# Optimization experiments

Measured on AMD Instinct MI355X. Metric: run time of the kernel, lower is better.

The kernel has to match this reference:

```python
import jax, jax.numpy as jnp
import numpy as np

GAMMA = 2.6
SIG0, SIG1 = 0.17, 4.86
EXP_S, EXP_F = 2.0, 0.6

F1_NP = np.array([[0.0025, 0.0125, 0.02, 0.0125, 0.0025],
                  [0.0125, 0.0625, 0.1, 0.0625, 0.0125],
                  [0.02, 0.1, 0.16, 0.1, 0.02],
                  [0.0125, 0.0625, 0.1, 0.0625, 0.0125],
                  [0.0025, 0.0125, 0.02, 0.0125, 0.0025]], dtype=np.float32)[None, None]
FILT0_NP = np.array([[0.04, 0.04, 0.05, 0.04, 0.04],
                     [0.04, 0.03, 0.04, 0.03, 0.04],
                     [0.05, 0.04, 0.05, 0.04, 0.05],
                     [0.04, 0.03, 0.04, 0.03, 0.04],
                     [0.04, 0.04, 0.05, 0.04, 0.04]], dtype=np.float32)[None, None]
FILT1_NP = np.zeros((5, 5), dtype=np.float32)
FILT1_NP[2, 2] = 1.0
FILT1_NP = FILT1_NP[None, None]


def _pad_rep(x, p):
    return jnp.pad(x, ((0, 0), (0, 0), (p, p), (p, p)), mode='edge')


def _conv(x, f, pad=0):
    return jax.lax.conv_general_dilated(
        x, f, window_strides=(1, 1), padding=[(pad, pad), (pad, pad)],
        dimension_numbers=('NCHW', 'OIHW', 'NCHW'))


def _down(img, f):
    # replicate-pad by 2, valid 5x5 conv (output same HxW), stride-2 subsample
    o = _conv(_pad_rep(img, 2), f)
    return o[:, :, ::2, ::2]


def _up(img, odd, f):
    x = _pad_rep(img, 1)
    B, C, Hp, Wp = x.shape
    h, w = 2 * Hp, 2 * Wp
    o = jnp.zeros((B, C, h, w), x.dtype).at[:, :, ::2, ::2].set(4.0 * x)
    o = _conv(o, f, pad=2)
    return o[:, :, 2:h - 2 - odd[0], 2:w - 2 - odd[1]]


def _laplacian_pyramid(img, n_lev, f):
    pyr = []
    o = img
    for _ in range(n_lev - 1):
        g = _down(o, f)
        odd = [g.shape[2] * 2 - o.shape[2], g.shape[3] * 2 - o.shape[3]]
        pyr.append(o - _up(g, odd, f))
        o = g
    pyr.append(o)
    return pyr


def _nlp(img, n_lev, F1, filt0, filt1):
    img = img ** (1.0 / GAMMA)
    pyr = _laplacian_pyramid(img, n_lev, F1)
    npyr = []
    for i in range(n_lev - 1):
        den = _conv(_pad_rep(jnp.abs(pyr[i]), 2), filt0) + SIG0
        npyr.append(pyr[i] / den)
    den = _conv(_pad_rep(jnp.abs(pyr[-1]), 2), filt1) + SIG1
    npyr.append(pyr[-1] / den)
    return npyr


def setup_inputs() -> dict:
    key = jax.random.key(0)
    k1, k2 = jax.random.split(key)
    B, H, W = 16, 512, 512
    h_img = jax.random.uniform(k1, (B, 1, H, W), dtype=jnp.float32)
    l_img = jax.random.uniform(k2, (B, 1, H, W), dtype=jnp.float32)
    return {
        'h_img': h_img,
        'l_img': l_img,
        'F1': jnp.asarray(F1_NP),
        'filt0': jnp.asarray(FILT0_NP),
        'filt1': jnp.asarray(FILT1_NP),
        'n_lev': 7,
    }


def reference(h_img, l_img, F1, filt0, filt1, n_lev):
    h_pyr = _nlp(h_img, n_lev, F1, filt0, filt1)
    l_pyr = _nlp(l_img, n_lev, F1, filt0, filt1)
    dis = []
    for i in range(n_lev):
        diff = jnp.abs(h_pyr[i] - l_pyr[i]) ** EXP_S
        dis.append(jnp.mean(diff, axis=(-2, -1)) ** (EXP_F / EXP_S))  # [B, 1]
    dis = jnp.concatenate(dis, axis=-1)  # [B, n_lev]
    loss = jnp.mean(dis, axis=-1) ** (1.0 / EXP_F)
    return jnp.mean(loss)
```

## Files before the change

kernel.cpp:

```cpp
#include <hip/hip_runtime.h>

#define SIG0 0.17f
#define SIG1 4.86f

__device__ __constant__ float c_filt0[25] = {
  0.04f,0.04f,0.05f,0.04f,0.04f,
  0.04f,0.03f,0.04f,0.03f,0.04f,
  0.05f,0.04f,0.05f,0.04f,0.05f,
  0.04f,0.03f,0.04f,0.03f,0.04f,
  0.04f,0.04f,0.05f,0.04f,0.04f};
__device__ __constant__ float c_f1d[5] = {0.05f,0.25f,0.4f,0.25f,0.05f};

static __device__ __forceinline__ int iclamp(int v, int lo, int hi){
  return v < lo ? lo : (v > hi ? hi : v);
}

#define D0W 136
#define D0H 36
__global__ __launch_bounds__(256)
void down0_gamma(const float* __restrict__ hin, const float* __restrict__ lin,
                 float* __restrict__ g0, float* __restrict__ g1){
  const int H=512, W=512, Wo=256;
  int xo0 = blockIdx.x*64, yo0 = blockIdx.y*16;
  int z = blockIdx.z;
  const float* in = (z<16) ? (hin + (size_t)z*H*W) : (lin + (size_t)(z-16)*H*W);
  int tid = threadIdx.x;
  __shared__ float st[D0H][D0W];
  __shared__ float hs[D0H][64];
  const float e = 0.3846153846153846f;
  for (int f=tid; f<D0H*D0W; f+=256){
    int r=f/D0W, c=f%D0W;
    int yy=iclamp(2*yo0-2+r,0,H-1);
    int xx=iclamp(2*xo0-4+c,0,W-1);
    st[r][c] = __powf(in[(size_t)yy*W+xx], e);
  }
  __syncthreads();
  float* g0p = g0 + (size_t)z*H*W;
  for (int f=tid; f<32*32; f+=256){
    int r=f>>5, q=f&31;
    float4 v = *(const float4*)&st[2+r][4+4*q];
    *(float4*)&g0p[(size_t)(2*yo0+r)*W + 2*xo0 + 4*q] = v;
  }
  for (int f=tid; f<D0H*64; f+=256){
    int r=f>>6, xo=f&63;
    const float* rp = &st[r][2*xo+2];
    hs[r][xo] = 0.05f*rp[0]+0.25f*rp[1]+0.4f*rp[2]+0.25f*rp[3]+0.05f*rp[4];
  }
  __syncthreads();
  float* g1p = g1 + (size_t)z*Wo*Wo;
  for (int f=tid; f<16*64; f+=256){
    int yo=f>>6, xo=f&63;
    g1p[(size_t)(yo0+yo)*Wo + xo0+xo] =
      0.05f*hs[2*yo][xo]+0.25f*hs[2*yo+1][xo]+0.4f*hs[2*yo+2][xo]
     +0.25f*hs[2*yo+3][xo]+0.05f*hs[2*yo+4][xo];
  }
}

#define DTW 132
#define DTH 36
__global__ __launch_bounds__(256)
void down_kernel(const float* __restrict__ in, float* __restrict__ out,
                 int H, int W, int Ho, int Wo){
  int xo0 = blockIdx.x*64, yo0 = blockIdx.y*16, b = blockIdx.z;
  int tid = threadIdx.x;
  __shared__ float st[DTH][DTW];
  __shared__ float hs[DTH][64];
  const float* ip = in + (size_t)b*H*W;
  for (int f = tid; f < DTH*DTW; f += 256){
    int r = f / DTW, c = f % DTW;
    int yy = iclamp(2*yo0 - 2 + r, 0, H-1);
    int xx = iclamp(2*xo0 - 2 + c, 0, W-1);
    st[r][c] = ip[(size_t)yy*W + xx];
  }
  __syncthreads();
  for (int f = tid; f < DTH*64; f += 256){
    int r = f >> 6, xo = f & 63;
    const float* rp = st[r] + 2*xo;
    hs[r][xo] = 0.05f*rp[0] + 0.25f*rp[1] + 0.4f*rp[2] + 0.25f*rp[3] + 0.05f*rp[4];
  }
  __syncthreads();
  for (int f = tid; f < 16*64; f += 256){
    int yo = f >> 6, xo = f & 63;
    int X = xo0 + xo, Y = yo0 + yo;
    if (X < Wo && Y < Ho){
      out[(size_t)b*Ho*Wo + (size_t)Y*Wo + X] =
        0.05f*hs[2*yo][xo] + 0.25f*hs[2*yo+1][xo] + 0.4f*hs[2*yo+2][xo]
      + 0.25f*hs[2*yo+3][xo] + 0.05f*hs[2*yo+4][xo];
    }
  }
}

#define FTW 72
#define FTH 20
#define FGW 40
#define FGH 12

static __device__ __forceinline__ float4 rowi(const float* p){
  float4 t;
  t.x = 0.05f*p[0] + 0.4f*p[1] + 0.05f*p[2];
  t.y = 0.25f*(p[1]+p[2]);
  t.z = 0.05f*p[1] + 0.4f*p[2] + 0.05f*p[3];
  t.w = 0.25f*(p[2]+p[3]);
  return t;
}

__global__ __launch_bounds__(256)
void fused_kernel(const float* __restrict__ g0, const float* __restrict__ g1,
                  float* __restrict__ accum, int H, int W, int lev){
  int Hg=H>>1, Wg=W>>1;
  int x0 = blockIdx.x*64, y0 = blockIdx.y*16, b = blockIdx.z;
  int tid = threadIdx.x;
  bool edge = (blockIdx.x==0) || (blockIdx.x==gridDim.x-1) ||
              (blockIdx.y==0) || (blockIdx.y==gridDim.y-1);

  __shared__ float sg[2][FTH][FTW];
  __shared__ float s1[2][FGH][FGW];
  __shared__ float swave[4];

  const float* g0b0 = g0 + (size_t)b*H*W;
  const float* g0b1 = g0 + (size_t)(b+16)*H*W;
  const float* g1b0 = g1 + (size_t)b*Hg*Wg;
  const float* g1b1 = g1 + (size_t)(b+16)*Hg*Wg;
  int gy0 = (y0>>1)-2, gx0 = (x0>>1)-4;

  if (!edge){
    for (int f=tid; f<2*FTH*18; f+=256){
      int img=f/360, rem=f%360, r=rem/18, q=rem%18;
      const float* src = img ? g0b1 : g0b0;
      *(float4*)&sg[img][r][4*q] = *(const float4*)&src[(size_t)(y0-2+r)*W + x0-4+4*q];
    }
    for (int f=tid; f<2*FGH*10; f+=256){
      int img=f/120, rem=f%120, r=rem/10, q=rem%10;
      const float* src = img ? g1b1 : g1b0;
      *(float4*)&s1[img][r][4*q] = *(const float4*)&src[(size_t)(gy0+r)*Wg + gx0+4*q];
    }
    __syncthreads();
    for (int f=tid; f<2*FTH*18; f+=256){
      int img=f/360, rem=f%360, r=rem/18, q=rem%18;
      int ry = ((r-2)>>1) + 2;
      int cb = 2*q+1;
      float4 u;
      if ((r&1)==0){
        float4 a = rowi(&s1[img][ry-1][cb]);
        float4 m = rowi(&s1[img][ry  ][cb]);
        float4 c2 = rowi(&s1[img][ry+1][cb]);
        u.x = 0.2f*a.x + 1.6f*m.x + 0.2f*c2.x;
        u.y = 0.2f*a.y + 1.6f*m.y + 0.2f*c2.y;
        u.z = 0.2f*a.z + 1.6f*m.z + 0.2f*c2.z;
        u.w = 0.2f*a.w + 1.6f*m.w + 0.2f*c2.w;
      } else {
        float4 a = rowi(&s1[img][ry  ][cb]);
        float4 m = rowi(&s1[img][ry+1][cb]);
        u.x = a.x + m.x; u.y = a.y + m.y; u.z = a.z + m.z; u.w = a.w + m.w;
      }
      float4 val = *(float4*)&sg[img][r][4*q];
      val.x -= u.x; val.y -= u.y; val.z -= u.z; val.w -= u.w;
      *(float4*)&sg[img][r][4*q] = val;
    }
  } else {
    for (int f=tid; f<2*FTH*FTW; f+=256){
      int img=f/(FTH*FTW), rem=f%(FTH*FTW), r=rem/FTW, c=rem%FTW;
      int yy=iclamp(y0-2+r,0,H-1), xx=iclamp(x0-4+c,0,W-1);
      const float* src = img ? g0b1 : g0b0;
      sg[img][r][c] = src[(size_t)yy*W+xx];
    }
    for (int f=tid; f<2*FGH*FGW; f+=256){
      int img=f/(FGH*FGW), rem=f%(FGH*FGW), r=rem/FGW, c=rem%FGW;
      int yy=iclamp(gy0+r,0,Hg-1), xx=iclamp(gx0+c,0,Wg-1);
      const float* src = img ? g1b1 : g1b0;
      s1[img][r][c] = src[(size_t)yy*Wg+xx];
    }
    __syncthreads();
    for (int f=tid; f<2*FTH*FTW; f+=256){
      int img=f/(FTH*FTW), rem=f%(FTH*FTW), r=rem/FTW, c=rem%FTW;
      int yy=iclamp(y0-2+r,0,H-1), xx=iclamp(x0-4+c,0,W-1);
      int y2=yy>>1, x2=xx>>1;
      int ry0,ry1,ry2; float wy0,wy1,wy2;
      if ((yy&1)==0){
        ry0=iclamp(y2-1,0,Hg-1); ry1=y2; ry2=iclamp(y2+1,0,Hg-1);
        wy0=0.2f; wy1=1.6f; wy2=0.2f;
      } else {
        ry0=y2; ry1=iclamp(y2+1,0,Hg-1); ry2=y2;
        wy0=1.0f; wy1=1.0f; wy2=0.0f;
      }
      int cx0,cx1,cx2; float wx0,wx1,wx2;
      if ((xx&1)==0){
        cx0=iclamp(x2-1,0,Wg-1); cx1=x2; cx2=iclamp(x2+1,0,Wg-1);
        wx0=0.05f; wx1=0.4f; wx2=0.05f;
      } else {
        cx0=x2; cx1=iclamp(x2+1,0,Wg-1); cx2=x2;
        wx0=0.25f; wx1=0.25f; wx2=0.0f;
      }
      ry0-=gy0; ry1-=gy0; ry2-=gy0; cx0-=gx0; cx1-=gx0; cx2-=gx0;
      const float (*sp)[FGW] = s1[img];
      float u0 = wx0*sp[ry0][cx0] + wx1*sp[ry0][cx1] + wx2*sp[ry0][cx2];
      float u1 = wx0*sp[ry1][cx0] + wx1*sp[ry1][cx1] + wx2*sp[ry1][cx2];
      float u2 = wx0*sp[ry2][cx0] + wx1*sp[ry2][cx1] + wx2*sp[ry2][cx2];
      sg[img][r][c] -= wy0*u0 + wy1*u1 + wy2*u2;
    }
  }
  __syncthreads();

  int tx = tid & 15, ty = tid >> 4;
  int xl = tx*4;
  float denh[4], denl[4], numh[4], numl[4];
  #pragma unroll
  for (int j=0;j<4;j++){ denh[j]=SIG0; denl[j]=SIG0; }
  #pragma unroll
  for (int i=0;i<5;i++){
    float r_[12];
    *(float4*)&r_[0] = *(const float4*)&sg[0][ty+i][xl];
    *(float4*)&r_[4] = *(const float4*)&sg[0][ty+i][xl+4];
    *(float4*)&r_[8] = *(const float4*)&sg[0][ty+i][xl+8];
    if (i==2){ numh[0]=r_[4]; numh[1]=r_[5]; numh[2]=r_[6]; numh[3]=r_[7]; }
    #pragma unroll
    for (int jj=0;jj<5;jj++){
      float w = c_filt0[i*5+jj];
      #pragma unroll
      for (int j=0;j<4;j++) denh[j] += w*fabsf(r_[2+j+jj]);
    }
  }
  #pragma unroll
  for (int i=0;i<5;i++){
    float r_[12];
    *(float4*)&r_[0] = *(const float4*)&sg[1][ty+i][xl];
    *(float4*)&r_[4] = *(const float4*)&sg[1][ty+i][xl+4];
    *(float4*)&r_[8] = *(const float4*)&sg[1][ty+i][xl+8];
    if (i==2){ numl[0]=r_[4]; numl[1]=r_[5]; numl[2]=r_[6]; numl[3]=r_[7]; }
    #pragma unroll
    for (int jj=0;jj<5;jj++){
      float w = c_filt0[i*5+jj];
      #pragma unroll
      for (int j=0;j<4;j++) denl[j] += w*fabsf(r_[2+j+jj]);
    }
  }
  float v = 0.f;
  #pragma unroll
  for (int j=0;j<4;j++){
    float d = __fdividef(numh[j], denh[j]) - __fdividef(numl[j], denl[j]);
    v += d*d;
  }
  #pragma unroll
  for (int off=32; off>0; off>>=1) v += __shfl_down(v, off);
  if ((tid & 63) == 0) swave[tid>>6] = v;
  __syncthreads();
  if (tid == 0){
    float s = swave[0]+swave[1]+swave[2]+swave[3];
    atomicAdd(&accum[lev*16 + b], s);
  }
}

static __device__ __forceinline__ void down_lds(const float* Ain, int ldi, int Sin,
                                                float* Aout, int ldo, int Sout,
                                                int tid, int NT){
  int tot = 2*Sout*Sout;
  for (int f=tid; f<tot; f+=NT){
    int img = f/(Sout*Sout), rem = f%(Sout*Sout), y=rem/Sout, x=rem%Sout;
    const float* A = Ain + img*Sin*ldi;
    float s=0.f;
    #pragma unroll
    for (int i=0;i<5;i++){
      int yy=iclamp(2*y+i-2,0,Sin-1);
      float rs=0.f;
      #pragma unroll
      for (int j=0;j<5;j++){
        int xx=iclamp(2*x+j-2,0,Sin-1);
        rs += c_f1d[j]*A[yy*ldi+xx];
      }
      s += c_f1d[i]*rs;
    }
    Aout[img*Sout*ldo + y*ldo + x] = s;
  }
}

static __device__ __forceinline__ void lap_lds(float* Ak, int ldk, int S,
                                               const float* Ag, int ldg,
                                               int tid, int NT){
  int Sg = S>>1;
  int tot = 2*S*S;
  for (int f=tid; f<tot; f+=NT){
    int img=f/(S*S), rem=f%(S*S), y=rem/S, x=rem%S;
    const float* G = Ag + img*Sg*ldg;
    int y2=y>>1, x2=x>>1;
    int ry0,ry1,ry2; float wy0,wy1,wy2;
    if (!(y&1)){ ry0=iclamp(y2-1,0,Sg-1); ry1=y2; ry2=iclamp(y2+1,0,Sg-1); wy0=0.2f; wy1=1.6f; wy2=0.2f; }
    else { ry0=y2; ry1=iclamp(y2+1,0,Sg-1); ry2=y2; wy0=1.f; wy1=1.f; wy2=0.f; }
    int cx0,cx1,cx2; float wx0,wx1,wx2;
    if (!(x&1)){ cx0=iclamp(x2-1,0,Sg-1); cx1=x2; cx2=iclamp(x2+1,0,Sg-1); wx0=0.05f; wx1=0.4f; wx2=0.05f; }
    else { cx0=x2; cx1=iclamp(x2+1,0,Sg-1); cx2=x2; wx0=0.25f; wx1=0.25f; wx2=0.f; }
    float u0 = wx0*G[ry0*ldg+cx0]+wx1*G[ry0*ldg+cx1]+wx2*G[ry0*ldg+cx2];
    float u1 = wx0*G[ry1*ldg+cx0]+wx1*G[ry1*ldg+cx1]+wx2*G[ry1*ldg+cx2];
    float u2 = wx0*G[ry2*ldg+cx0]+wx1*G[ry2*ldg+cx1]+wx2*G[ry2*ldg+cx2];
    Ak[img*S*ldk + y*ldk + x] -= wy0*u0+wy1*u1+wy2*u2;
  }
}

static __device__ __forceinline__ float diff_lds(const float* A, int ld, int S,
                                                 int tid, int NT){
  float v=0.f;
  const float* Ah = A;
  const float* Al = A + S*ld;
  for (int f=tid; f<S*S; f+=NT){
    int y=f/S, x=f%S;
    float dh=SIG0, dl=SIG0;
    #pragma unroll
    for (int i=0;i<5;i++){
      int yy=iclamp(y+i-2,0,S-1);
      #pragma unroll
      for (int j=0;j<5;j++){
        int xx=iclamp(x+j-2,0,S-1);
        float w=c_filt0[i*5+j];
        dh += w*fabsf(Ah[yy*ld+xx]);
        dl += w*fabsf(Al[yy*ld+xx]);
      }
    }
    float d = __fdividef(Ah[y*ld+x],dh) - __fdividef(Al[y*ld+x],dl);
    v += d*d;
  }
  return v;
}

__global__ __launch_bounds__(512)
void tail_kernel(const float* __restrict__ g3, float* __restrict__ accum){
  const int NT = 512;
  int b = blockIdx.x;
  int tid = threadIdx.x;
  __shared__ float A3[2][64][66];
  __shared__ float A4[2][32][34];
  __shared__ float A5[2][16][18];
  __shared__ float A6[2][8][10];
  __shared__ float sred[8];

  const float* s0 = g3 + (size_t)b*4096;
  const float* s1p = g3 + (size_t)(b+16)*4096;
  for (int f=tid; f<2*4096; f+=NT){
    int img=f>>12, rem=f&4095, r=rem>>6, c=rem&63;
    A3[img][r][c] = img ? s1p[rem] : s0[rem];
  }
  __syncthreads();
  down_lds(&A3[0][0][0], 66, 64, &A4[0][0][0], 34, 32, tid, NT);
  __syncthreads();
  down_lds(&A4[0][0][0], 34, 32, &A5[0][0][0], 18, 16, tid, NT);
  __syncthreads();
  down_lds(&A5[0][0][0], 18, 16, &A6[0][0][0], 10, 8, tid, NT);
  __syncthreads();
  lap_lds(&A3[0][0][0], 66, 64, &A4[0][0][0], 34, tid, NT);
  __syncthreads();
  float v3 = diff_lds(&A3[0][0][0], 66, 64, tid, NT);
  lap_lds(&A4[0][0][0], 34, 32, &A5[0][0][0], 18, tid, NT);
  __syncthreads();
  float v4 = diff_lds(&A4[0][0][0], 34, 32, tid, NT);
  lap_lds(&A5[0][0][0], 18, 16, &A6[0][0][0], 10, tid, NT);
  __syncthreads();
  float v5 = diff_lds(&A5[0][0][0], 18, 16, tid, NT);
  float v6 = 0.f;
  for (int f=tid; f<64; f+=NT){
    float ch = A6[0][f>>3][f&7];
    float cl = A6[1][f>>3][f&7];
    float d = __fdividef(ch, fabsf(ch)+SIG1) - __fdividef(cl, fabsf(cl)+SIG1);
    v6 += d*d;
  }
  float vs[4] = {v3, v4, v5, v6};
  #pragma unroll
  for (int k=0;k<4;k++){
    float v = vs[k];
    #pragma unroll
    for (int off=32; off>0; off>>=1) v += __shfl_down(v, off);
    if ((tid&63)==0) sred[tid>>6] = v;
    __syncthreads();
    if (tid==0){
      float s=0.f;
      #pragma unroll
      for (int w=0;w<8;w++) s += sred[w];
      accum[(3+k)*16 + b] = s;
    }
    __syncthreads();
  }
}

__global__ __launch_bounds__(64)
void finalize_kernel(const float* __restrict__ accum, float* __restrict__ out){
  __shared__ float s[16];
  int b = threadIdx.x;
  if (b < 16){
    float m = 0.f;
    #pragma unroll
    for (int k=0;k<7;k++){
      int hw = (512>>k)*(512>>k);
      float mean = accum[k*16+b] / (float)hw;
      m += powf(mean, 0.3f);
    }
    m *= (1.0f/7.0f);
    s[b] = powf(m, 1.6666666666666667f);
  }
  __syncthreads();
  if (b == 0){
    float t = 0.f;
    #pragma unroll
    for (int i=0;i<16;i++) t += s[i];
    out[0] = t * (1.0f/16.0f);
  }
}

extern "C" void kernel_launch(void* const* d_in, const int* in_sizes, int n_in,
                              void* d_out, int out_size, void* d_ws, size_t ws_size,
                              hipStream_t stream){
  const float* h = (const float*)d_in[0];
  const float* l = (const float*)d_in[1];
  float* out = (float*)d_out;
  float* ws = (float*)d_ws;

  size_t off0 = 0;
  size_t off1 = off0 + (size_t)32*512*512;
  size_t off2 = off1 + (size_t)32*256*256;
  size_t off3 = off2 + (size_t)32*128*128;
  size_t offA = off3 + (size_t)32*64*64;
  float* accum = ws + offA;

  hipMemsetAsync(accum, 0, 112*sizeof(float), stream);

  down0_gamma<<<dim3(4,16,32), 256, 0, stream>>>(h, l, ws+off0, ws+off1);
  fused_kernel<<<dim3(8,32,16), 256, 0, stream>>>(ws+off0, ws+off1, accum, 512, 512, 0);
  down_kernel<<<dim3(2,8,32), 256, 0, stream>>>(ws+off1, ws+off2, 256, 256, 128, 128);
  fused_kernel<<<dim3(4,16,16), 256, 0, stream>>>(ws+off1, ws+off2, accum, 256, 256, 1);
  down_kernel<<<dim3(1,4,32), 256, 0, stream>>>(ws+off2, ws+off3, 128, 128, 64, 64);
  fused_kernel<<<dim3(2,8,16), 256, 0, stream>>>(ws+off2, ws+off3, accum, 128, 128, 2);
  tail_kernel<<<dim3(16), 512, 0, stream>>>(ws+off3, accum);
  finalize_kernel<<<1, 64, 0, stream>>>(accum, out);
}
```

Baseline: 195.5 us.

## Fuse pyramid stages into fewer launches with pre-padded buffers and recomputed level0

Drops the full-resolution gamma-corrected buffer g0 and recomputes the gamma power from the inputs inside the level-0 Laplacian kernel. Downsampled levels are stored with replicated-edge padding, so the fused kernels need no clamped slow path. Each downsample is merged into the same launch as the previous level's Laplacian/normalisation work using blockIdx.z partitioning, cutting the launch count from eight to five. Fused tiles grow to 32 rows, each thread computing two output rows. The cost is redundant pow evaluations, scattered halo writes and larger shared memory per block.

```diff
diff --git a/kernel.cpp b/kernel.cpp
--- a/kernel.cpp
+++ b/kernel.cpp
@@ -15,239 +15,244 @@
   return v < lo ? lo : (v > hi ? hi : v);
 }
 
-#define D0W 136
-#define D0H 36
-__global__ __launch_bounds__(256)
-void down0_gamma(const float* __restrict__ hin, const float* __restrict__ lin,
-                 float* __restrict__ g0, float* __restrict__ g1){
-  const int H=512, W=512, Wo=256;
-  int xo0 = blockIdx.x*64, yo0 = blockIdx.y*16;
-  int z = blockIdx.z;
-  const float* in = (z<16) ? (hin + (size_t)z*H*W) : (lin + (size_t)(z-16)*H*W);
-  int tid = threadIdx.x;
-  __shared__ float st[D0H][D0W];
-  __shared__ float hs[D0H][64];
-  const float e = 0.3846153846153846f;
-  for (int f=tid; f<D0H*D0W; f+=256){
-    int r=f/D0W, c=f%D0W;
-    int yy=iclamp(2*yo0-2+r,0,H-1);
-    int xx=iclamp(2*xo0-4+c,0,W-1);
-    st[r][c] = __powf(in[(size_t)yy*W+xx], e);
-  }
-  __syncthreads();
-  float* g0p = g0 + (size_t)z*H*W;
-  for (int f=tid; f<32*32; f+=256){
-    int r=f>>5, q=f&31;
-    float4 v = *(const float4*)&st[2+r][4+4*q];
-    *(float4*)&g0p[(size_t)(2*yo0+r)*W + 2*xo0 + 4*q] = v;
-  }
-  for (int f=tid; f<D0H*64; f+=256){
+
+struct FS {
+  float sg[2][36][76];
+  float s1[2][20][44];
+  float red[4];
+};
+struct DS {
+  float st[36][136];
+  float hs[36][64];
+};
+struct TS {
+  float A3[2][64][66];
+  float A4[2][32][34];
+  float A5[2][16][18];
+  float A6[2][8][10];
+  float red[4];
+};
+
+__device__ __forceinline__ void down_body(const float* __restrict__ in0, float* __restrict__ out0,
+                                          int PSI, int PSO, int Sout, int xo0, int yo0, char* smem){
+  DS* S = (DS*)smem;
+  int tid = threadIdx.x;
+  for (int f=tid; f<36*34; f+=256){
+    int r=f/34, c4=f%34;
+    *(float4*)&S->st[r][4*c4] = *(const float4*)&in0[(size_t)(2*yo0+r)*PSI + 2*xo0 + 4*c4];
+  }
+  __syncthreads();
+  for (int f=tid; f<36*64; f+=256){
     int r=f>>6, xo=f&63;
-    const float* rp = &st[r][2*xo+2];
-    hs[r][xo] = 0.05f*rp[0]+0.25f*rp[1]+0.4f*rp[2]+0.25f*rp[3]+0.05f*rp[4];
-  }
-  __syncthreads();
-  float* g1p = g1 + (size_t)z*Wo*Wo;
+    const float* rp = &S->st[r][2*xo+2];
+    S->hs[r][xo] = 0.05f*rp[0]+0.25f*rp[1]+0.4f*rp[2]+0.25f*rp[3]+0.05f*rp[4];
+  }
+  __syncthreads();
   for (int f=tid; f<16*64; f+=256){
     int yo=f>>6, xo=f&63;
-    g1p[(size_t)(yo0+yo)*Wo + xo0+xo] =
-      0.05f*hs[2*yo][xo]+0.25f*hs[2*yo+1][xo]+0.4f*hs[2*yo+2][xo]
-     +0.25f*hs[2*yo+3][xo]+0.05f*hs[2*yo+4][xo];
-  }
-}
-
-#define DTW 132
-#define DTH 36
+    int Y=yo0+yo, X=xo0+xo;
+    float v = 0.05f*S->hs[2*yo][xo]+0.25f*S->hs[2*yo+1][xo]+0.4f*S->hs[2*yo+2][xo]
+            +0.25f*S->hs[2*yo+3][xo]+0.05f*S->hs[2*yo+4][xo];
+    int rlo=(Y==0)?0:(Y+2), rhi=(Y==Sout-1)?(Sout+3):(Y+2);
+    int clo=(X==0)?0:(X+4), chi=(X==Sout-1)?(Sout+7):(X+4);
+    for (int rr=rlo; rr<=rhi; rr++)
+      for (int cc=clo; cc<=chi; cc++)
+        out0[(size_t)rr*PSO+cc] = v;
+  }
+}
+
 __global__ __launch_bounds__(256)
-void down_kernel(const float* __restrict__ in, float* __restrict__ out,
-                 int H, int W, int Ho, int Wo){
-  int xo0 = blockIdx.x*64, yo0 = blockIdx.y*16, b = blockIdx.z;
-  int tid = threadIdx.x;
-  __shared__ float st[DTH][DTW];
-  __shared__ float hs[DTH][64];
-  const float* ip = in + (size_t)b*H*W;
-  for (int f = tid; f < DTH*DTW; f += 256){
-    int r = f / DTW, c = f % DTW;
-    int yy = iclamp(2*yo0 - 2 + r, 0, H-1);
-    int xx = iclamp(2*xo0 - 2 + c, 0, W-1);
-    st[r][c] = ip[(size_t)yy*W + xx];
-  }
-  __syncthreads();
-  for (int f = tid; f < DTH*64; f += 256){
-    int r = f >> 6, xo = f & 63;
-    const float* rp = st[r] + 2*xo;
-    hs[r][xo] = 0.05f*rp[0] + 0.25f*rp[1] + 0.4f*rp[2] + 0.25f*rp[3] + 0.05f*rp[4];
-  }
-  __syncthreads();
-  for (int f = tid; f < 16*64; f += 256){
-    int yo = f >> 6, xo = f & 63;
-    int X = xo0 + xo, Y = yo0 + yo;
-    if (X < Wo && Y < Ho){
-      out[(size_t)b*Ho*Wo + (size_t)Y*Wo + X] =
-        0.05f*hs[2*yo][xo] + 0.25f*hs[2*yo+1][xo] + 0.4f*hs[2*yo+2][xo]
-      + 0.25f*hs[2*yo+3][xo] + 0.05f*hs[2*yo+4][xo];
-    }
-  }
-}
-
-#define FTW 72
-#define FTH 20
-#define FGW 40
-#define FGH 12
-
-static __device__ __forceinline__ float4 rowi(const float* p){
+void k_d1(const float* __restrict__ hin, const float* __restrict__ lin,
+          float* __restrict__ g1){
+  __shared__ DS S;
+  int xo0 = blockIdx.x*64, yo0 = blockIdx.y*16, z = blockIdx.z;
+  const float* in = (z<16)? hin + (size_t)z*262144 : lin + (size_t)(z-16)*262144;
+  float* out0 = g1 + (size_t)z*68640;
+  int tid = threadIdx.x;
+  const float e = 0.3846153846153846f;
+  for (int f=tid; f<36*34; f+=256){
+    int r=f/34, c4=f%34;
+    int yy = iclamp(2*yo0-2+r, 0, 511);
+    int xb = 2*xo0-4+4*c4;
+    const float* rp = in + (size_t)yy*512;
+    float4 v;
+    if (xb>=0 && xb<=508) v = *(const float4*)&rp[xb];
+    else { v.x=rp[iclamp(xb,0,511)]; v.y=rp[iclamp(xb+1,0,511)];
+           v.z=rp[iclamp(xb+2,0,511)]; v.w=rp[iclamp(xb+3,0,511)]; }
+    v.x=__powf(v.x,e); v.y=__powf(v.y,e); v.z=__powf(v.z,e); v.w=__powf(v.w,e);
+    *(float4*)&S.st[r][4*c4] = v;
+  }
+  __syncthreads();
+  for (int f=tid; f<36*64; f+=256){
+    int r=f>>6, xo=f&63;
+    const float* rp = &S.st[r][2*xo+2];
+    S.hs[r][xo] = 0.05f*rp[0]+0.25f*rp[1]+0.4f*rp[2]+0.25f*rp[3]+0.05f*rp[4];
+  }
+  __syncthreads();
+  for (int f=tid; f<16*64; f+=256){
+    int yo=f>>6, xo=f&63;
+    int Y=yo0+yo, X=xo0+xo;
+    float v = 0.05f*S.hs[2*yo][xo]+0.25f*S.hs[2*yo+1][xo]+0.4f*S.hs[2*yo+2][xo]
+            +0.25f*S.hs[2*yo+3][xo]+0.05f*S.hs[2*yo+4][xo];
+    int rlo=(Y==0)?0:(Y+2), rhi=(Y==255)?259:(Y+2);
+    int clo=(X==0)?0:(X+4), chi=(X==255)?263:(X+4);
+    for (int rr=rlo; rr<=rhi; rr++)
+      for (int cc=clo; cc<=chi; cc++)
+        out0[(size_t)rr*264+cc] = v;
+  }
+}
+
+__device__ __forceinline__ void fused_stage_s1(FS* S, const float* __restrict__ g10,
+                                               const float* __restrict__ g11,
+                                               int PS1, int x0, int y0){
+  int tid = threadIdx.x;
+  for (int f=tid; f<2*20*10; f+=256){
+    int img=f/200, rem=f%200, ro=rem/10, co=rem%10;
+    const float* src = img? g11 : g10;
+    *(float4*)&S->s1[img][ro][4*co] = *(const float4*)&src[(size_t)(y0/2+ro)*PS1 + x0/2 + 4*co];
+  }
+}
+
+__device__ __forceinline__ void fused_stage_g(FS* S, const float* __restrict__ gk0,
+                                              const float* __restrict__ gk1,
+                                              int PS0, int x0, int y0){
+  int tid = threadIdx.x;
+  for (int f=tid; f<2*36*18; f+=256){
+    int img=f/648, rem=f%648, r=rem/18, q=rem%18;
+    const float* src = img? gk1 : gk0;
+    *(float4*)&S->sg[img][r][4*q] = *(const float4*)&src[(size_t)(y0+r)*PS0 + x0 + 4*q];
+  }
+}
+
+__device__ __forceinline__ void fused_stage_in(FS* S, const float* __restrict__ h0,
+                                               const float* __restrict__ l0,
+                                               int x0, int y0){
+  int tid = threadIdx.x;
+  const float e = 0.3846153846153846f;
+  for (int f=tid; f<2*36*18; f+=256){
+    int img=f/648, rem=f%648, r=rem/18, q=rem%18;
+    const float* src = img? l0 : h0;
+    int yy = iclamp(y0-2+r, 0, 511);
+    int xb = x0-4+4*q;
+    const float* rp = src + (size_t)yy*512;
+    float4 v;
+    if (xb>=0 && xb<=508) v = *(const float4*)&rp[xb];
+    else { v.x=rp[iclamp(xb,0,511)]; v.y=rp[iclamp(xb+1,0,511)];
+           v.z=rp[iclamp(xb+2,0,511)]; v.w=rp[iclamp(xb+3,0,511)]; }
+    v.x=__powf(v.x,e); v.y=__powf(v.y,e); v.z=__powf(v.z,e); v.w=__powf(v.w,e);
+    *(float4*)&S->sg[img][r][4*q] = v;
+  }
+}
+
+__device__ __forceinline__ float4 up_row(const float* __restrict__ p){
+  float2 A = *(const float2*)p;
+  float2 B = *(const float2*)(p+2);
+  float2 C = *(const float2*)(p+4);
   float4 t;
-  t.x = 0.05f*p[0] + 0.4f*p[1] + 0.05f*p[2];
-  t.y = 0.25f*(p[1]+p[2]);
-  t.z = 0.05f*p[1] + 0.4f*p[2] + 0.05f*p[3];
-  t.w = 0.25f*(p[2]+p[3]);
+  t.x = 0.05f*A.y + 0.4f*B.x + 0.05f*B.y;
+  t.y = 0.25f*(B.x+B.y);
+  t.z = 0.05f*B.x + 0.4f*B.y + 0.05f*C.x;
+  t.w = 0.25f*(B.y+C.x);
   return t;
 }
 
-__global__ __launch_bounds__(256)
-void fused_kernel(const float* __restrict__ g0, const float* __restrict__ g1,
-                  float* __restrict__ accum, int H, int W, int lev){
-  int Hg=H>>1, Wg=W>>1;
-  int x0 = blockIdx.x*64, y0 = blockIdx.y*16, b = blockIdx.z;
-  int tid = threadIdx.x;
-  bool edge = (blockIdx.x==0) || (blockIdx.x==gridDim.x-1) ||
-              (blockIdx.y==0) || (blockIdx.y==gridDim.y-1);
-
-  __shared__ float sg[2][FTH][FTW];
-  __shared__ float s1[2][FGH][FGW];
-  __shared__ float swave[4];
-
-  const float* g0b0 = g0 + (size_t)b*H*W;
-  const float* g0b1 = g0 + (size_t)(b+16)*H*W;
-  const float* g1b0 = g1 + (size_t)b*Hg*Wg;
-  const float* g1b1 = g1 + (size_t)(b+16)*Hg*Wg;
-  int gy0 = (y0>>1)-2, gx0 = (x0>>1)-4;
-
-  if (!edge){
-    for (int f=tid; f<2*FTH*18; f+=256){
-      int img=f/360, rem=f%360, r=rem/18, q=rem%18;
-      const float* src = img ? g0b1 : g0b0;
-      *(float4*)&sg[img][r][4*q] = *(const float4*)&src[(size_t)(y0-2+r)*W + x0-4+4*q];
-    }
-    for (int f=tid; f<2*FGH*10; f+=256){
-      int img=f/120, rem=f%120, r=rem/10, q=rem%10;
-      const float* src = img ? g1b1 : g1b0;
-      *(float4*)&s1[img][r][4*q] = *(const float4*)&src[(size_t)(gy0+r)*Wg + gx0+4*q];
+__device__ __forceinline__ void fused_tail(FS* S, int Simg, int x0, int y0,
+                                           float* __restrict__ accum, int lev, int b){
+  int tid = threadIdx.x;
+  __syncthreads();
+
+  for (int f=tid; f<2*36*18; f+=256){
+    int img=f/648, rem=f%648, r=rem/18, q=rem%18;
+    int ry = ((r-2)>>1)+2;
+    int cq = 2*q;
+    float4 u;
+    if ((r&1)==0){
+      float4 a = up_row(&S->s1[img][ry-1][cq]);
+      float4 m = up_row(&S->s1[img][ry  ][cq]);
+      float4 c2= up_row(&S->s1[img][ry+1][cq]);
+      u.x = 0.2f*a.x+1.6f*m.x+0.2f*c2.x;
+      u.y = 0.2f*a.y+1.6f*m.y+0.2f*c2.y;
+      u.z = 0.2f*a.z+1.6f*m.z+0.2f*c2.z;
+      u.w = 0.2f*a.w+1.6f*m.w+0.2f*c2.w;
+    } else {
+      float4 a = up_row(&S->s1[img][ry  ][cq]);
+      float4 m = up_row(&S->s1[img][ry+1][cq]);
+      u.x=a.x+m.x; u.y=a.y+m.y; u.z=a.z+m.z; u.w=a.w+m.w;
+    }
+    float4 val = *(float4*)&S->sg[img][r][4*q];
+    val.x-=u.x; val.y-=u.y; val.z-=u.z; val.w-=u.w;
+    *(float4*)&S->sg[img][r][4*q] = val;
+  }
+  __syncthreads();
+
+  bool top=(y0==0), bot=(y0+32==Simg), lft=(x0==0), rgt=(x0+64==Simg);
+  if (top||bot||lft||rgt){
+    for (int f=tid; f<2*18; f+=256){
+      int img=f/18, q=f%18;
+      if (top){ float4 v=*(float4*)&S->sg[img][2][4*q];
+                *(float4*)&S->sg[img][0][4*q]=v; *(float4*)&S->sg[img][1][4*q]=v; }
+      if (bot){ float4 v=*(float4*)&S->sg[img][33][4*q];
+                *(float4*)&S->sg[img][34][4*q]=v; *(float4*)&S->sg[img][35][4*q]=v; }
     }
     __syncthreads();
-    for (int f=tid; f<2*FTH*18; f+=256){
-      int img=f/360, rem=f%360, r=rem/18, q=rem%18;
-      int ry = ((r-2)>>1) + 2;
-      int cb = 2*q+1;
-      float4 u;
-      if ((r&1)==0){
-        float4 a = rowi(&s1[img][ry-1][cb]);
-        float4 m = rowi(&s1[img][ry  ][cb]);
-        float4 c2 = rowi(&s1[img][ry+1][cb]);
-        u.x = 0.2f*a.x + 1.6f*m.x + 0.2f*c2.x;
-        u.y = 0.2f*a.y + 1.6f*m.y + 0.2f*c2.y;
-        u.z = 0.2f*a.z + 1.6f*m.z + 0.2f*c2.z;
-        u.w = 0.2f*a.w + 1.6f*m.w + 0.2f*c2.w;
-      } else {
-        float4 a = rowi(&s1[img][ry  ][cb]);
-        float4 m = rowi(&s1[img][ry+1][cb]);
-        u.x = a.x + m.x; u.y = a.y + m.y; u.z = a.z + m.z; u.w = a.w + m.w;
+    for (int f=tid; f<2*36; f+=256){
+      int img=f/36, r=f%36;
+      if (lft){ float v=S->sg[img][r][4];  float4 vv={v,v,v,v}; *(float4*)&S->sg[img][r][0]=vv; }
+      if (rgt){ float v=S->sg[img][r][67]; float4 vv={v,v,v,v}; *(float4*)&S->sg[img][r][68]=vv; }
+    }
+    __syncthreads();
+  }
+
+  int tx = tid & 15, ty = tid >> 4;
+  int xl = 4*tx;
+  float vacc = 0.f;
+  float q0o0[4], q0o1[4];
+  #pragma unroll
+  for (int img=0; img<2; img++){
+    float d0[4]={SIG0,SIG0,SIG0,SIG0}, d1[4]={SIG0,SIG0,SIG0,SIG0};
+    float n0[4], n1[4];
+    #pragma unroll
+    for (int i=0;i<6;i++){
+      float r_[12];
+      *(float4*)&r_[0] = *(const float4*)&S->sg[img][2*ty+i][xl];
+      *(float4*)&r_[4] = *(const float4*)&S->sg[img][2*ty+i][xl+4];
+      *(float4*)&r_[8] = *(const float4*)&S->sg[img][2*ty+i][xl+8];
+      if (i==2){ n0[0]=r_[4]; n0[1]=r_[5]; n0[2]=r_[6]; n0[3]=r_[7]; }
+      if (i==3){ n1[0]=r_[4]; n1[1]=r_[5]; n1[2]=r_[6]; n1[3]=r_[7]; }
+      if (i<5){
+        #pragma unroll
+        for (int jj=0;jj<5;jj++){
+          float w = c_filt0[i*5+jj];
+          #pragma unroll
+          for (int j=0;j<4;j++) d0[j] += w*fabsf(r_[2+j+jj]);
+        }
       }
-      float4 val = *(float4*)&sg[img][r][4*q];
-      val.x -= u.x; val.y -= u.y; val.z -= u.z; val.w -= u.w;
-      *(float4*)&sg[img][r][4*q] = val;
-    }
-  } else {
-    for (int f=tid; f<2*FTH*FTW; f+=256){
-      int img=f/(FTH*FTW), rem=f%(FTH*FTW), r=rem/FTW, c=rem%FTW;
-      int yy=iclamp(y0-2+r,0,H-1), xx=iclamp(x0-4+c,0,W-1);
-      const float* src = img ? g0b1 : g0b0;
-      sg[img][r][c] = src[(size_t)yy*W+xx];
-    }
-    for (int f=tid; f<2*FGH*FGW; f+=256){
-      int img=f/(FGH*FGW), rem=f%(FGH*FGW), r=rem/FGW, c=rem%FGW;
-      int yy=iclamp(gy0+r,0,Hg-1), xx=iclamp(gx0+c,0,Wg-1);
-      const float* src = img ? g1b1 : g1b0;
-      s1[img][r][c] = src[(size_t)yy*Wg+xx];
-    }
-    __syncthreads();
-    for (int f=tid; f<2*FTH*FTW; f+=256){
-      int img=f/(FTH*FTW), rem=f%(FTH*FTW), r=rem/FTW, c=rem%FTW;
-      int yy=iclamp(y0-2+r,0,H-1), xx=iclamp(x0-4+c,0,W-1);
-      int y2=yy>>1, x2=xx>>1;
-      int ry0,ry1,ry2; float wy0,wy1,wy2;
-      if ((yy&1)==0){
-        ry0=iclamp(y2-1,0,Hg-1); ry1=y2; ry2=iclamp(y2+1,0,Hg-1);
-        wy0=0.2f; wy1=1.6f; wy2=0.2f;
-      } else {
-        ry0=y2; ry1=iclamp(y2+1,0,Hg-1); ry2=y2;
-        wy0=1.0f; wy1=1.0f; wy2=0.0f;
+      if (i>0){
+        #pragma unroll
+        for (int jj=0;jj<5;jj++){
+          float w = c_filt0[(i-1)*5+jj];
+          #pragma unroll
+          for (int j=0;j<4;j++) d1[j] += w*fabsf(r_[2+j+jj]);
+        }
       }
-      int cx0,cx1,cx2; float wx0,wx1,wx2;
-      if ((xx&1)==0){
-        cx0=iclamp(x2-1,0,Wg-1); cx1=x2; cx2=iclamp(x2+1,0,Wg-1);
-        wx0=0.05f; wx1=0.4f; wx2=0.05f;
-      } else {
-        cx0=x2; cx1=iclamp(x2+1,0,Wg-1); cx2=x2;
-        wx0=0.25f; wx1=0.25f; wx2=0.0f;
+    }
+    if (img==0){
+      #pragma unroll
+      for (int j=0;j<4;j++){ q0o0[j]=__fdividef(n0[j],d0[j]); q0o1[j]=__fdividef(n1[j],d1[j]); }
+    } else {
+      #pragma unroll
+      for (int j=0;j<4;j++){
+        float a = q0o0[j]-__fdividef(n0[j],d0[j]); vacc += a*a;
+        float b2= q0o1[j]-__fdividef(n1[j],d1[j]); vacc += b2*b2;
       }
-      ry0-=gy0; ry1-=gy0; ry2-=gy0; cx0-=gx0; cx1-=gx0; cx2-=gx0;
-      const float (*sp)[FGW] = s1[img];
-      float u0 = wx0*sp[ry0][cx0] + wx1*sp[ry0][cx1] + wx2*sp[ry0][cx2];
-      float u1 = wx0*sp[ry1][cx0] + wx1*sp[ry1][cx1] + wx2*sp[ry1][cx2];
-      float u2 = wx0*sp[ry2][cx0] + wx1*sp[ry2][cx1] + wx2*sp[ry2][cx2];
-      sg[img][r][c] -= wy0*u0 + wy1*u1 + wy2*u2;
-    }
-  }
-  __syncthreads();
-
-  int tx = tid & 15, ty = tid >> 4;
-  int xl = tx*4;
-  float denh[4], denl[4], numh[4], numl[4];
+    }
+  }
   #pragma unroll
-  for (int j=0;j<4;j++){ denh[j]=SIG0; denl[j]=SIG0; }
-  #pragma unroll
-  for (int i=0;i<5;i++){
-    float r_[12];
-    *(float4*)&r_[0] = *(const float4*)&sg[0][ty+i][xl];
-    *(float4*)&r_[4] = *(const float4*)&sg[0][ty+i][xl+4];
-    *(float4*)&r_[8] = *(const float4*)&sg[0][ty+i][xl+8];
-    if (i==2){ numh[0]=r_[4]; numh[1]=r_[5]; numh[2]=r_[6]; numh[3]=r_[7]; }
-    #pragma unroll
-    for (int jj=0;jj<5;jj++){
-      float w = c_filt0[i*5+jj];
-      #pragma unroll
-      for (int j=0;j<4;j++) denh[j] += w*fabsf(r_[2+j+jj]);
-    }
-  }
-  #pragma unroll
-  for (int i=0;i<5;i++){
-    float r_[12];
-    *(float4*)&r_[0] = *(const float4*)&sg[1][ty+i][xl];
-    *(float4*)&r_[4] = *(const float4*)&sg[1][ty+i][xl+4];
-    *(float4*)&r_[8] = *(const float4*)&sg[1][ty+i][xl+8];
-    if (i==2){ numl[0]=r_[4]; numl[1]=r_[5]; numl[2]=r_[6]; numl[3]=r_[7]; }
-    #pragma unroll
-    for (int jj=0;jj<5;jj++){
-      float w = c_filt0[i*5+jj];
-      #pragma unroll
-      for (int j=0;j<4;j++) denl[j] += w*fabsf(r_[2+j+jj]);
-    }
-  }
-  float v = 0.f;
-  #pragma unroll
-  for (int j=0;j<4;j++){
-    float d = __fdividef(numh[j], denh[j]) - __fdividef(numl[j], denl[j]);
-    v += d*d;
-  }
-  #pragma unroll
-  for (int off=32; off>0; off>>=1) v += __shfl_down(v, off);
-  if ((tid & 63) == 0) swave[tid>>6] = v;
-  __syncthreads();
-  if (tid == 0){
-    float s = swave[0]+swave[1]+swave[2]+swave[3];
-    atomicAdd(&accum[lev*16 + b], s);
-  }
+  for (int off=32; off>0; off>>=1) vacc += __shfl_down(vacc, off);
+  if ((tid&63)==0) S->red[tid>>6] = vacc;
+  __syncthreads();
+  if (tid==0)
+    atomicAdd(&accum[lev*16+b], S->red[0]+S->red[1]+S->red[2]+S->red[3]);
 }
 
 static __device__ __forceinline__ void down_lds(const float* Ain, int ldi, int Sin,
@@ -320,43 +325,36 @@
   return v;
 }
 
-__global__ __launch_bounds__(512)
-void tail_kernel(const float* __restrict__ g3, float* __restrict__ accum){
-  const int NT = 512;
-  int b = blockIdx.x;
-  int tid = threadIdx.x;
-  __shared__ float A3[2][64][66];
-  __shared__ float A4[2][32][34];
-  __shared__ float A5[2][16][18];
-  __shared__ float A6[2][8][10];
-  __shared__ float sred[8];
-
-  const float* s0 = g3 + (size_t)b*4096;
-  const float* s1p = g3 + (size_t)(b+16)*4096;
-  for (int f=tid; f<2*4096; f+=NT){
+__device__ void tail_body(const float* __restrict__ g3, float* __restrict__ accum,
+                          int b, char* smem){
+  TS* T = (TS*)smem;
+  int tid = threadIdx.x;
+  const float* s0  = g3 + (size_t)b*4896 + 148;
+  const float* s1p = g3 + (size_t)(b+16)*4896 + 148;
+  for (int f=tid; f<2*4096; f+=256){
     int img=f>>12, rem=f&4095, r=rem>>6, c=rem&63;
-    A3[img][r][c] = img ? s1p[rem] : s0[rem];
-  }
-  __syncthreads();
-  down_lds(&A3[0][0][0], 66, 64, &A4[0][0][0], 34, 32, tid, NT);
-  __syncthreads();
-  down_lds(&A4[0][0][0], 34, 32, &A5[0][0][0], 18, 16, tid, NT);
-  __syncthreads();
-  down_lds(&A5[0][0][0], 18, 16, &A6[0][0][0], 10, 8, tid, NT);
-  __syncthreads();
-  lap_lds(&A3[0][0][0], 66, 64, &A4[0][0][0], 34, tid, NT);
-  __syncthreads();
-  float v3 = diff_lds(&A3[0][0][0], 66, 64, tid, NT);
-  lap_lds(&A4[0][0][0], 34, 32, &A5[0][0][0], 18, tid, NT);
-  __syncthreads();
-  float v4 = diff_lds(&A4[0][0][0], 34, 32, tid, NT);
-  lap_lds(&A5[0][0][0], 18, 16, &A6[0][0][0], 10, tid, NT);
-  __syncthreads();
-  float v5 = diff_lds(&A5[0][0][0], 18, 16, tid, NT);
+    T->A3[img][r][c] = (img? s1p : s0)[(size_t)r*72+c];
+  }
+  __syncthreads();
+  down_lds(&T->A3[0][0][0],66,64,&T->A4[0][0][0],34,32,tid,256);
+  __syncthreads();
+  down_lds(&T->A4[0][0][0],34,32,&T->A5[0][0][0],18,16,tid,256);
+  __syncthreads();
+  down_lds(&T->A5[0][0][0],18,16,&T->A6[0][0][0],10,8,tid,256);
+  __syncthreads();
+  lap_lds(&T->A3[0][0][0],66,64,&T->A4[0][0][0],34,tid,256);
+  __syncthreads();
+  float v3 = diff_lds(&T->A3[0][0][0],66,64,tid,256);
+  lap_lds(&T->A4[0][0][0],34,32,&T->A5[0][0][0],18,tid,256);
+  __syncthreads();
+  float v4 = diff_lds(&T->A4[0][0][0],34,32,tid,256);
+  lap_lds(&T->A5[0][0][0],18,16,&T->A6[0][0][0],10,tid,256);
+  __syncthreads();
+  float v5 = diff_lds(&T->A5[0][0][0],18,16,tid,256);
   float v6 = 0.f;
-  for (int f=tid; f<64; f+=NT){
-    float ch = A6[0][f>>3][f&7];
-    float cl = A6[1][f>>3][f&7];
+  for (int f=tid; f<64; f+=256){
+    float ch = T->A6[0][f>>3][f&7];
+    float cl = T->A6[1][f>>3][f&7];
     float d = __fdividef(ch, fabsf(ch)+SIG1) - __fdividef(cl, fabsf(cl)+SIG1);
     v6 += d*d;
   }
@@ -366,20 +364,68 @@
     float v = vs[k];
     #pragma unroll
     for (int off=32; off>0; off>>=1) v += __shfl_down(v, off);
-    if ((tid&63)==0) sred[tid>>6] = v;
+    if ((tid&63)==0) T->red[tid>>6] = v;
     __syncthreads();
     if (tid==0){
-      float s=0.f;
-      #pragma unroll
-      for (int w=0;w<8;w++) s += sred[w];
-      accum[(3+k)*16 + b] = s;
+      accum[(3+k)*16 + b] = T->red[0]+T->red[1]+T->red[2]+T->red[3];
     }
     __syncthreads();
   }
 }
 
+__global__ __launch_bounds__(256)
+void k_d2(const float* __restrict__ h, const float* __restrict__ l,
+          const float* __restrict__ g1, float* __restrict__ g2,
+          float* __restrict__ accum){
+  extern __shared__ char smem[];
+  if (blockIdx.z < 16){
+    FS* S = (FS*)smem;
+    int b = blockIdx.z, x0 = blockIdx.x*64, y0 = blockIdx.y*32;
+    fused_stage_in(S, h+(size_t)b*262144, l+(size_t)b*262144, x0, y0);
+    fused_stage_s1(S, g1+(size_t)b*68640, g1+(size_t)(b+16)*68640, 264, x0, y0);
+    fused_tail(S, 512, x0, y0, accum, 0, b);
+  } else {
+    int id = (blockIdx.z-16)*128 + blockIdx.y*8 + blockIdx.x;
+    int db = id>>4, dby = (id>>1)&7, dbx = id&1;
+    down_body(g1+(size_t)db*68640, g2+(size_t)db*17952, 264, 136, 128, dbx*64, dby*16, smem);
+  }
+}
+
+__global__ __launch_bounds__(256)
+void k_d4(const float* __restrict__ g1, float* __restrict__ g2,
+          float* __restrict__ g3, float* __restrict__ accum){
+  extern __shared__ char smem[];
+  if (blockIdx.z < 16){
+    FS* S = (FS*)smem;
+    int b = blockIdx.z, x0 = blockIdx.x*64, y0 = blockIdx.y*32;
+    fused_stage_g(S, g1+(size_t)b*68640, g1+(size_t)(b+16)*68640, 264, x0, y0);
+    fused_stage_s1(S, g2+(size_t)b*17952, g2+(size_t)(b+16)*17952, 136, x0, y0);
+    fused_tail(S, 256, x0, y0, accum, 1, b);
+  } else {
+    int id = (blockIdx.z-16)*32 + blockIdx.y*4 + blockIdx.x;
+    int db = id>>2, dby = id&3;
+    down_body(g2+(size_t)db*17952, g3+(size_t)db*4896, 136, 72, 64, 0, dby*16, smem);
+  }
+}
+
+__global__ __launch_bounds__(256)
+void k_d5(const float* __restrict__ g2, const float* __restrict__ g3,
+          float* __restrict__ accum){
+  extern __shared__ char smem[];
+  if (blockIdx.z < 16){
+    FS* S = (FS*)smem;
+    int b = blockIdx.z, x0 = blockIdx.x*64, y0 = blockIdx.y*32;
+    fused_stage_g(S, g2+(size_t)b*17952, g2+(size_t)(b+16)*17952, 136, x0, y0);
+    fused_stage_s1(S, g3+(size_t)b*4896, g3+(size_t)(b+16)*4896, 72, x0, y0);
+    fused_tail(S, 128, x0, y0, accum, 2, b);
+  } else {
+    int id = (blockIdx.z-16)*8 + blockIdx.y*2 + blockIdx.x;
+    tail_body(g3, accum, id, smem);
+  }
+}
+
 __global__ __launch_bounds__(64)
-void finalize_kernel(const float* __restrict__ accum, float* __restrict__ out){
+void k_d6(const float* __restrict__ accum, float* __restrict__ out){
   __shared__ float s[16];
   int b = threadIdx.x;
   if (b < 16){
@@ -410,21 +456,16 @@
   float* out = (float*)d_out;
   float* ws = (float*)d_ws;
 
-  size_t off0 = 0;
-  size_t off1 = off0 + (size_t)32*512*512;
-  size_t off2 = off1 + (size_t)32*256*256;
-  size_t off3 = off2 + (size_t)32*128*128;
-  size_t offA = off3 + (size_t)32*64*64;
-  float* accum = ws + offA;
+  float* g1 = ws;
+  float* g2 = g1 + 2196480;
+  float* g3 = g2 + 574464;
+  float* accum = g3 + 156672;
 
   hipMemsetAsync(accum, 0, 112*sizeof(float), stream);
 
-  down0_gamma<<<dim3(4,16,32), 256, 0, stream>>>(h, l, ws+off0, ws+off1);
-  fused_kernel<<<dim3(8,32,16), 256, 0, stream>>>(ws+off0, ws+off1, accum, 512, 512, 0);
-  down_kernel<<<dim3(2,8,32), 256, 0, stream>>>(ws+off1, ws+off2, 256, 256, 128, 128);
-  fused_kernel<<<dim3(4,16,16), 256, 0, stream>>>(ws+off1, ws+off2, accum, 256, 256, 1);
-  down_kernel<<<dim3(1,4,32), 256, 0, stream>>>(ws+off2, ws+off3, 128, 128, 64, 64);
-  fused_kernel<<<dim3(2,8,16), 256, 0, stream>>>(ws+off2, ws+off3, accum, 128, 128, 2);
-  tail_kernel<<<dim3(16), 512, 0, stream>>>(ws+off3, accum);
-  finalize_kernel<<<1, 64, 0, stream>>>(accum, out);
-}
+  k_d1<<<dim3(4,16,32), 256, 0, stream>>>(h, l, g1);
+  k_d2<<<dim3(8,16,20), 256, sizeof(FS), stream>>>(h, l, g1, g2, accum);
+  k_d4<<<dim3(4,8,20),  256, sizeof(FS), stream>>>(g1, g2, g3, accum);
+  k_d5<<<dim3(2,4,18),  256, sizeof(TS), stream>>>(g2, g3, accum);
+  k_d6<<<1, 64, 0, stream>>>(accum, out);
+}
```

After: 174.3 us. 1.12x faster.
